# Kernel tuning notes

Hardware: AMD Instinct MI355X
Metric: run time of the kernel (lower is better)

## Reference

```python
import jax, jax.numpy as jnp
import numpy as np

B, S, L2 = 1, 2048, 512
DIM, HEADS, HD, FFN = 1536, 12, 128, 8960
BLK, TOPK, EPS = 64, 8, 1e-6
SCALE = HD ** -0.5

def _ln(x):
    xc = x - jnp.mean(x, -1, keepdims=True)
    return xc * jax.lax.rsqrt(jnp.mean(xc * xc, -1, keepdims=True) + EPS)

def _rms(x, w):
    return x * jax.lax.rsqrt(jnp.mean(x * x, -1, keepdims=True) + EPS) * w

def _rope(x, cos, sin):
    # is_neox_style=False: interleaved pairs
    x1, x2 = x[..., 0::2], x[..., 1::2]
    c, s = cos[None, :, None, :], sin[None, :, None, :]
    return jnp.stack([x1 * c - x2 * s, x2 * c + x1 * s], -1).reshape(x.shape)

def forward(hidden_states, encoder_hidden_states, temb, cos, sin, scale_shift_table,
            Wq, bq, Wk, bk, Wv, bv, Wg, bg, Wo, bo, qnorm_w, knorm_w, sa_ln_w, sa_ln_b,
            cWq, cbq, cWk, cbk, cWv, cbv, cWo, cbo, cqnorm_w, cknorm_w, W1, b1, W2, b2):
    e = scale_shift_table + temb  # [B,6,DIM]
    shift_msa, scale_msa, gate_msa = e[:, 0:1], e[:, 1:2], e[:, 2:3]
    c_shift, c_scale, c_gate = e[:, 3:4], e[:, 4:5], e[:, 5:6]
    norm_hs = _ln(hidden_states) * (1.0 + scale_msa) + shift_msa
    q = _rms(norm_hs @ Wq + bq, qnorm_w).reshape(B, S, HEADS, HD)
    k = _rms(norm_hs @ Wk + bk, knorm_w).reshape(B, S, HEADS, HD)
    v = (norm_hs @ Wv + bv).reshape(B, S, HEADS, HD)
    g = (norm_hs @ Wg + bg).reshape(B, S, HEADS, HD)  # gate_compress
    q, k = _rope(q, cos, sin), _rope(k, cos, sin)
    # ---- Video Sparse Attention: coarse (gated) branch + block top-k fine branch ----
    nb = S // BLK
    qc = q.reshape(B, nb, BLK, HEADS, HD).mean(2)  # cube-pooled
    kc = k.reshape(B, nb, BLK, HEADS, HD).mean(2)
    vc = v.reshape(B, nb, BLK, HEADS, HD).mean(2)
    pc = jax.nn.softmax(jnp.einsum('bnhd,bmhd->bhnm', qc, kc) * SCALE, -1)
    coarse = jnp.repeat(jnp.einsum('bhnm,bmhd->bnhd', pc, vc), BLK, axis=1)  # [B,S,H,D]
    _, idx = jax.lax.top_k(pc, TOPK)  # [B,H,nb,TOPK] selected kv blocks
    blk_mask = jax.nn.one_hot(idx, nb, dtype=jnp.float32).sum(-2) > 0  # [B,H,nb,nb]
    tok_mask = jnp.repeat(jnp.repeat(blk_mask, BLK, 2), BLK, 3)  # [B,H,S,S]
    s_fine = jnp.einsum('bshd,bthd->bhst', q, k) * SCALE
    p = jax.nn.softmax(jnp.where(tok_mask, s_fine, -1e9), -1)
    fine = jnp.einsum('bhst,bthd->bshd', p, v)
    attn = (fine + g * coarse).reshape(B, S, DIM) @ Wo + bo
    # ---- ScaleResidualLayerNormScaleShift (affine LN, null shift/scale) ----
    res = hidden_states + gate_msa * attn
    norm2 = _ln(res) * sa_ln_w + sa_ln_b
    # ---- WanT2VCrossAttention ----
    cq = _rms(norm2 @ cWq + cbq, cqnorm_w).reshape(B, S, HEADS, HD)
    ck = _rms(encoder_hidden_states @ cWk + cbk, cknorm_w).reshape(B, L2, HEADS, HD)
    cv = (encoder_hidden_states @ cWv + cbv).reshape(B, L2, HEADS, HD)
    cp = jax.nn.softmax(jnp.einsum('bshd,bthd->bhst', cq, ck) * SCALE, -1)
    cross = jnp.einsum('bhst,bthd->bshd', cp, cv).reshape(B, S, DIM) @ cWo + cbo
    res2 = res + cross
    norm3 = _ln(res2) * (1.0 + c_scale) + c_shift  # non-affine LN + scale-shift
    # ---- gelu-tanh MLP + gated residual ----
    ff = jax.nn.gelu(norm3 @ W1 + b1, approximate=True) @ W2 + b2
    return res2 + c_gate * ff

def setup_inputs():
    key = jax.random.key(0)
    ks = jax.random.split(key, 16)
    def w(i, shape, s=0.02):
        return jax.random.normal(ks[i], shape, jnp.float32) * s
    ang = jnp.arange(S, dtype=jnp.float32)[:, None] / (10000.0 ** (jnp.arange(0, HD, 2, dtype=jnp.float32) / HD))[None, :]
    z = lambda n: jnp.zeros((n,), jnp.float32)
    o = lambda n: jnp.ones((n,), jnp.float32)
    return {
        'hidden_states': jax.random.normal(ks[0], (B, S, DIM), jnp.float32),
        'encoder_hidden_states': jax.random.normal(ks[1], (B, L2, DIM), jnp.float32),
        'temb': jax.random.normal(ks[2], (B, 6, DIM), jnp.float32),
        'cos': jnp.cos(ang), 'sin': jnp.sin(ang),
        'scale_shift_table': jax.random.normal(ks[3], (1, 6, DIM), jnp.float32) / DIM ** 0.5,
        'Wq': w(4, (DIM, DIM)), 'bq': z(DIM), 'Wk': w(5, (DIM, DIM)), 'bk': z(DIM),
        'Wv': w(6, (DIM, DIM)), 'bv': z(DIM), 'Wg': w(7, (DIM, DIM)), 'bg': z(DIM),
        'Wo': w(8, (DIM, DIM)), 'bo': z(DIM),
        'qnorm_w': o(DIM), 'knorm_w': o(DIM), 'sa_ln_w': o(DIM), 'sa_ln_b': z(DIM),
        'cWq': w(9, (DIM, DIM)), 'cbq': z(DIM), 'cWk': w(10, (DIM, DIM)), 'cbk': z(DIM),
        'cWv': w(11, (DIM, DIM)), 'cbv': z(DIM), 'cWo': w(12, (DIM, DIM)), 'cbo': z(DIM),
        'cqnorm_w': o(DIM), 'cknorm_w': o(DIM),
        'W1': w(13, (DIM, FFN)), 'b1': z(FFN), 'W2': w(14, (FFN, DIM)), 'b2': z(DIM),
    }

def reference(hidden_states, encoder_hidden_states, temb, cos, sin, scale_shift_table, Wq, bq, Wk, bk, Wv, bv, Wg, bg, Wo, bo, qnorm_w, knorm_w, sa_ln_w, sa_ln_b, cWq, cbq, cWk, cbk, cWv, cbv, cWo, cbo, cqnorm_w, cknorm_w, W1, b1, W2, b2):
    return forward(hidden_states, encoder_hidden_states, temb, cos, sin, scale_shift_table, Wq, bq, Wk, bk, Wv, bv, Wg, bg, Wo, bo, qnorm_w, knorm_w, sa_ln_w, sa_ln_b, cWq, cbq, cWk, cbk, cWv, cbv, cWo, cbo, cqnorm_w, cknorm_w, W1, b1, W2, b2)
```

## Files before the change

### kernel.cpp

```cpp
#include <hip/hip_runtime.h>
#include <hip/hip_bf16.h>
#include <math.h>

#define DIMX 1536
#define SEQ 2048
#define L2X 512
#define NHEAD 12
#define HDIM 128
#define NBLK 32
#define FFNX 8960
#define SCALE_ATT 0.08838834764831845f

typedef __attribute__((ext_vector_type(4))) float f4;
typedef __attribute__((ext_vector_type(4))) float f32x4;
typedef __attribute__((ext_vector_type(8))) short bf16x8;
typedef __attribute__((ext_vector_type(4))) unsigned short us4;
typedef __attribute__((ext_vector_type(8))) unsigned short us8;
typedef unsigned short us;

static __device__ __forceinline__ us f2bf(float f) {
  union { float f; unsigned u; } v; v.f = f;
  unsigned r = v.u + 0x7FFFu + ((v.u >> 16) & 1u);
  return (us)(r >> 16);
}

static __device__ __forceinline__ void gl_lds16(const us* g, us* l) {
  __builtin_amdgcn_global_load_lds(
      (const __attribute__((address_space(1))) void*)g,
      (__attribute__((address_space(3))) void*)l, 16, 0, 0);
}

#define RAW_BAR() asm volatile("s_barrier" ::: "memory")

static __device__ __forceinline__ void xcd_map2(int& bx, int& by) {
  int gx = gridDim.x, gy = gridDim.y;
  int nwg = gx * gy;
  int lin = by * gx + bx;
  int q = nwg >> 3;
  lin = (lin & 7) * q + (lin >> 3);
  bx = lin % gx;
  by = lin / gx;
}

__global__ void __launch_bounds__(256) prep_e_kernel(const float* __restrict__ sst,
                                                     const float* __restrict__ temb,
                                                     float* __restrict__ e) {
  int i = blockIdx.x * 256 + threadIdx.x;
  if (i < 6 * DIMX) e[i] = sst[i] + temb[i];
}

struct P9 { const float* s[9]; };

__global__ void __launch_bounds__(256) pack64_9(P9 ps, us* __restrict__ dst) {
  const float* __restrict__ W = ps.s[blockIdx.z];
  us* __restrict__ Wt = dst + (size_t)blockIdx.z * DIMX * DIMX;
  __shared__ float t[64][65];
  int n0 = blockIdx.x * 64, k0 = blockIdx.y * 64;
  int tid = threadIdx.x;
#pragma unroll
  for (int i = 0; i < 4; i++) {
    int c = i * 256 + tid;
    int row = c >> 4, c4 = (c & 15) * 4;
    *reinterpret_cast<f4*>(&t[row][c4]) =
        *reinterpret_cast<const f4*>(&W[(size_t)(k0 + row) * DIMX + n0 + c4]);
  }
  __syncthreads();
#pragma unroll
  for (int i = 0; i < 2; i++) {
    int c = i * 256 + tid;
    int n = c >> 3, kc = (c & 7) * 8;
    us8 h;
#pragma unroll
    for (int j = 0; j < 8; j++) h[j] = f2bf(t[kc + j][n]);
    *reinterpret_cast<us8*>(&Wt[(size_t)(n0 + n) * DIMX + k0 + kc]) = h;
  }
}

__global__ void __launch_bounds__(256) pack64_g(const float* __restrict__ W,
                                                us* __restrict__ Wt, int K, int N) {
  __shared__ float t[64][65];
  int n0 = blockIdx.x * 64, k0 = blockIdx.y * 64;
  int tid = threadIdx.x;
#pragma unroll
  for (int i = 0; i < 4; i++) {
    int c = i * 256 + tid;
    int row = c >> 4, c4 = (c & 15) * 4;
    *reinterpret_cast<f4*>(&t[row][c4]) =
        *reinterpret_cast<const f4*>(&W[(size_t)(k0 + row) * N + n0 + c4]);
  }
  __syncthreads();
#pragma unroll
  for (int i = 0; i < 2; i++) {
    int c = i * 256 + tid;
    int n = c >> 3, kc = (c & 7) * 8;
    us8 h;
#pragma unroll
    for (int j = 0; j < 8; j++) h[j] = f2bf(t[kc + j][n]);
    *reinterpret_cast<us8*>(&Wt[(size_t)(n0 + n) * K + k0 + kc]) = h;
  }
}

__global__ void __launch_bounds__(256) pack_cvt_kernel(const float* __restrict__ X,
                                                       us* __restrict__ Y, int n4) {
  int i = blockIdx.x * 256 + threadIdx.x;
  if (i < n4) {
    f4 v = *reinterpret_cast<const f4*>(&X[(size_t)i * 4]);
    us4 h; h[0] = f2bf(v[0]); h[1] = f2bf(v[1]); h[2] = f2bf(v[2]); h[3] = f2bf(v[3]);
    *reinterpret_cast<us4*>(&Y[(size_t)i * 4]) = h;
  }
}

__global__ void __launch_bounds__(256) ln_affine_kernel(
    const float* __restrict__ X, const float* __restrict__ a,
    const float* __restrict__ b, int add1, us* __restrict__ Out) {
  __shared__ float lds4[4];
  int row = blockIdx.x, t = threadIdx.x;
  const float* x = X + (size_t)row * DIMX;
  float v[6]; float s = 0.f;
#pragma unroll
  for (int i = 0; i < 6; i++) { v[i] = x[t + 256 * i]; s += v[i]; }
  for (int o = 1; o < 64; o <<= 1) s += __shfl_xor(s, o, 64);
  if ((t & 63) == 0) lds4[t >> 6] = s;
  __syncthreads();
  float mean = (lds4[0] + lds4[1] + lds4[2] + lds4[3]) * (1.f / DIMX);
  __syncthreads();
  float s2 = 0.f;
#pragma unroll
  for (int i = 0; i < 6; i++) { float c = v[i] - mean; s2 += c * c; }
  for (int o = 1; o < 64; o <<= 1) s2 += __shfl_xor(s2, o, 64);
  if ((t & 63) == 0) lds4[t >> 6] = s2;
  __syncthreads();
  float var = (lds4[0] + lds4[1] + lds4[2] + lds4[3]) * (1.f / DIMX);
  float rstd = rsqrtf(var + 1e-6f);
#pragma unroll
  for (int i = 0; i < 6; i++) {
    int c = t + 256 * i;
    float av = a[c] + (add1 ? 1.f : 0.f);
    Out[(size_t)row * DIMX + c] = f2bf((v[i] - mean) * rstd * av + b[c]);
  }
}

__global__ void __launch_bounds__(256) reduce_ln_kernel(
    const float* __restrict__ P, const float* __restrict__ bias,
    const float* __restrict__ R, const float* __restrict__ g,
    float* __restrict__ Ores, const float* __restrict__ a,
    const float* __restrict__ b, int add1, us* __restrict__ Onorm) {
  __shared__ float lds4[4];
  int row = blockIdx.x, t = threadIdx.x;
  const size_t RN = (size_t)SEQ * DIMX;
  float v[6]; float s = 0.f;
#pragma unroll
  for (int i = 0; i < 6; i++) {
    int c = t + 256 * i;
    size_t ix = (size_t)row * DIMX + c;
    float x = P[ix];
    x += P[RN + ix]; x += P[2 * RN + ix]; x += P[3 * RN + ix];
    x += bias[c];
    x = g ? (R[ix] + g[c] * x) : (R[ix] + x);
    Ores[ix] = x;
    v[i] = x; s += x;
  }
  for (int o = 1; o < 64; o <<= 1) s += __shfl_xor(s, o, 64);
  if ((t & 63) == 0) lds4[t >> 6] = s;
  __syncthreads();
  float mean = (lds4[0] + lds4[1] + lds4[2] + lds4[3]) * (1.f / DIMX);
  __syncthreads();
  float s2 = 0.f;
#pragma unroll
  for (int i = 0; i < 6; i++) { float c = v[i] - mean; s2 += c * c; }
  for (int o = 1; o < 64; o <<= 1) s2 += __shfl_xor(s2, o, 64);
  if ((t & 63) == 0) lds4[t >> 6] = s2;
  __syncthreads();
  float var = (lds4[0] + lds4[1] + lds4[2] + lds4[3]) * (1.f / DIMX);
  float rstd = rsqrtf(var + 1e-6f);
#pragma unroll
  for (int i = 0; i < 6; i++) {
    int c = t + 256 * i;
    float av = a[c] + (add1 ? 1.f : 0.f);
    Onorm[(size_t)row * DIMX + c] = f2bf((v[i] - mean) * rstd * av + b[c]);
  }
}

__global__ void __launch_bounds__(256) rms_rope2_kernel(
    float* __restrict__ X0, float* __restrict__ X1,
    const float* __restrict__ w0, const float* __restrict__ w1,
    const float* __restrict__ cosT, const float* __restrict__ sinT, int do_rope,
    us* __restrict__ O0, us* __restrict__ O1) {
  __shared__ float lds4[4];
  int row = blockIdx.x, t = threadIdx.x;
  float* x = (blockIdx.y ? X1 : X0) + (size_t)row * DIMX;
  const float* wgt = blockIdx.y ? w1 : w0;
  us* Ob = blockIdx.y ? O1 : O0;
  int base = t * 6;
  float v[6]; float s2 = 0.f;
#pragma unroll
  for (int i = 0; i < 6; i++) { v[i] = x[base + i]; s2 += v[i] * v[i]; }
  for (int o = 1; o < 64; o <<= 1) s2 += __shfl_xor(s2, o, 64);
  if ((t & 63) == 0) lds4[t >> 6] = s2;
  __syncthreads();
  float ms = (lds4[0] + lds4[1] + lds4[2] + lds4[3]) * (1.f / DIMX);
  float rstd = rsqrtf(ms + 1e-6f);
#pragma unroll
  for (int i = 0; i < 6; i++) v[i] *= rstd * wgt[base + i];
  if (do_rope) {
#pragma unroll
    for (int j = 0; j < 3; j++) {
      int c = base + 2 * j;
      int pi = (c & (HDIM - 1)) >> 1;
      float cs = cosT[row * (HDIM / 2) + pi], sn = sinT[row * (HDIM / 2) + pi];
      float ev = v[2 * j], ov = v[2 * j + 1];
      v[2 * j] = ev * cs - ov * sn;
      v[2 * j + 1] = ov * cs + ev * sn;
    }
  }
#pragma unroll
  for (int i = 0; i < 6; i++) {
    x[base + i] = v[i];
    Ob[(size_t)row * DIMX + base + i] = f2bf(v[i]);
  }
}

__global__ void __launch_bounds__(256) rms_rope_kernel(
    float* __restrict__ X, const float* __restrict__ wgt,
    const float* __restrict__ cosT, const float* __restrict__ sinT, int do_rope,
    us* __restrict__ Ob) {
  __shared__ float lds4[4];
  int row = blockIdx.x, t = threadIdx.x;
  float* x = X + (size_t)row * DIMX;
  int base = t * 6;
  float v[6]; float s2 = 0.f;
#pragma unroll
  for (int i = 0; i < 6; i++) { v[i] = x[base + i]; s2 += v[i] * v[i]; }
  for (int o = 1; o < 64; o <<= 1) s2 += __shfl_xor(s2, o, 64);
  if ((t & 63) == 0) lds4[t >> 6] = s2;
  __syncthreads();
  float ms = (lds4[0] + lds4[1] + lds4[2] + lds4[3]) * (1.f / DIMX);
  float rstd = rsqrtf(ms + 1e-6f);
#pragma unroll
  for (int i = 0; i < 6; i++) v[i] *= rstd * wgt[base + i];
  if (do_rope) {
#pragma unroll
    for (int j = 0; j < 3; j++) {
      int c = base + 2 * j;
      int pi = (c & (HDIM - 1)) >> 1;
      float cs = cosT[row * (HDIM / 2) + pi], sn = sinT[row * (HDIM / 2) + pi];
      float ev = v[2 * j], ov = v[2 * j + 1];
      v[2 * j] = ev * cs - ov * sn;
      v[2 * j + 1] = ov * cs + ev * sn;
    }
  }
#pragma unroll
  for (int i = 0; i < 6; i++) {
    x[base + i] = v[i];
    Ob[(size_t)row * DIMX + base + i] = f2bf(v[i]);
  }
}

struct Outs {
  float *o0, *o1, *o2, *o3;
  const float *b0, *b1, *b2, *b3;
  us* ob;
};

template<int NP, int NCHUNK, int OUT_BF16, int DO_GELU, int SPLITK, int DIRECT>
__global__ void __launch_bounds__(512, 2) gemm2ph(
    const us* __restrict__ A, const us* __restrict__ Bt,
    Outs outs, int M, int N, int K, int Kfull) {
  constexpr int NT = NP * 32;
  constexpr int TOT = 16384 + NT * 64;
  constexpr int BI = (NT * 8 + 511) / 512;
  constexpr int NH0 = NP / 2;
  constexpr int NH1 = NP - NH0;
  __shared__ __align__(16) us S[2 * TOT];
  const int tid = threadIdx.x;
  const int lane = tid & 63;
  const int wid = tid >> 6;
  const int wr = wid >> 1, wc = wid & 1;
  const int fr = lane & 15, xo = lane >> 4;
  const int r7 = fr & 7, q4 = xo * 4;
  int tm, tn;
  if (DIRECT) {
    tm = blockIdx.x * 256; tn = blockIdx.y * NT;
  } else {
    int bx = blockIdx.x, by = blockIdx.y;
    xcd_map2(bx, by);
    tm = by * 256; tn = bx * NT;
  }
  const size_t kb = SPLITK ? (size_t)blockIdx.z * K : 0;

  auto stA = [&](int buf, int k0) {
#pragma unroll
    for (int i = 0; i < 4; i++) {
      int c = i * 512 + tid;
      gl_lds16(A + (size_t)(tm + (c >> 3)) * Kfull + kb + k0 + (((c & 7) ^ ((c >> 3) & 7)) * 8),
               S + buf * TOT + (i * 512 + wid * 64) * 8);
    }
  };
  auto stB = [&](int buf, int k0) {
#pragma unroll
    for (int i = 0; i < BI; i++) {
      int c = i * 512 + tid;
      if (c < NT * 8)
        gl_lds16(Bt + (size_t)(tn + (c >> 3)) * Kfull + kb + k0 + (((c & 7) ^ ((c >> 3) & 7)) * 8),
                 S + buf * TOT + 16384 + (i * 512 + wid * 64) * 8);
    }
  };
  auto rdA = [&](int buf, int mp, int ks) -> bf16x8 {
    int r = wr * 64 + mp * 16 + fr;
    int ko = ((ks * 4 + xo) ^ r7) * 8;
    return *reinterpret_cast<const bf16x8*>(&S[buf * TOT + r * 64 + ko]);
  };
  auto rdB = [&](int buf, int np, int ks) -> bf16x8 {
    int r = wc * (NP * 16) + np * 16 + fr;
    int ko = ((ks * 4 + xo) ^ r7) * 8;
    return *reinterpret_cast<const bf16x8*>(&S[buf * TOT + 16384 + r * 64 + ko]);
  };

  f32x4 acc[4][NP];
#pragma unroll
  for (int m = 0; m < 4; m++)
#pragma unroll
    for (int n = 0; n < NP; n++) acc[m][n] = (f32x4)(0.f);
  bf16x8 aF[2][4], bFr[2][NH1 > NH0 ? NH1 : NH0];

  const int nt = K >> 6;
  stA(0, 0); stB(0, 0); stA(1, 64);
  asm volatile("s_waitcnt vmcnt(4)" ::: "memory");
  RAW_BAR();

  for (int t = 0; t < nt; t++) {
    const int buf = t & 1;
    const int k1 = (t + 1) << 6, k2 = (t + 2) << 6;
#pragma unroll
    for (int ks = 0; ks < 2; ks++)
#pragma unroll
      for (int m = 0; m < 4; m++) aF[ks][m] = rdA(buf, m, ks);
#pragma unroll
    for (int ks = 0; ks < 2; ks++)
#pragma unroll
      for (int n = 0; n < NH0; n++) bFr[ks][n] = rdB(buf, n, ks);
    if (t + 1 < nt) stB(buf ^ 1, k1);
    RAW_BAR();
    __builtin_amdgcn_s_setprio(1);
#pragma unroll
    for (int ks = 0; ks < 2; ks++)
#pragma unroll
      for (int m = 0; m < 4; m++)
#pragma unroll
        for (int n = 0; n < NH0; n++)
          acc[m][n] = __builtin_amdgcn_mfma_f32_16x16x32_bf16(aF[ks][m], bFr[ks][n], acc[m][n], 0, 0, 0);
    __builtin_amdgcn_s_setprio(0);
    RAW_BAR();
#pragma unroll
    for (int ks = 0; ks < 2; ks++)
#pragma unroll
      for (int n = 0; n < NH1; n++) bFr[ks][n] = rdB(buf, NH0 + n, ks);
    if (t + 2 < nt) stA(buf, k2);
    RAW_BAR();
    __builtin_amdgcn_s_setprio(1);
#pragma unroll
    for (int ks = 0; ks < 2; ks++)
#pragma unroll
      for (int m = 0; m < 4; m++)
#pragma unroll
        for (int n = 0; n < NH1; n++)
          acc[m][NH0 + n] = __builtin_amdgcn_mfma_f32_16x16x32_bf16(aF[ks][m], bFr[ks][n], acc[m][NH0 + n], 0, 0, 0);
    __builtin_amdgcn_s_setprio(0);
    if (t + 2 < nt) asm volatile("s_waitcnt vmcnt(4)" ::: "memory");
    else            asm volatile("s_waitcnt vmcnt(0)" ::: "memory");
    RAW_BAR();
  }

#pragma unroll
  for (int m = 0; m < 4; m++)
#pragma unroll
    for (int n = 0; n < NP; n++) {
      int col = tn + wc * (NP * 16) + n * 16 + fr;
      int rowb = tm + wr * 64 + m * 16 + q4;
      if (SPLITK) {
        float* P = outs.o0 + (size_t)blockIdx.z * M * N;
#pragma unroll
        for (int r = 0; r < 4; r++)
          P[(size_t)(rowb + r) * N + col] = acc[m][n][r];
      } else {
        int c2; float* op; const float* bp; int sel = 0;
        if constexpr (NCHUNK == 1) {
          c2 = col; op = outs.o0; bp = outs.b0;
        } else {
          sel = col >= 3 * DIMX ? 3 : (col >= 2 * DIMX ? 2 : (col >= DIMX ? 1 : 0));
          c2 = col - sel * DIMX;
          op = sel == 0 ? outs.o0 : (sel == 1 ? outs.o1 : (sel == 2 ? outs.o2 : outs.o3));
          bp = sel == 0 ? outs.b0 : (sel == 1 ? outs.b1 : (sel == 2 ? outs.b2 : outs.b3));
        }
        float bv = bp[c2];
#pragma unroll
        for (int r = 0; r < 4; r++) {
          float v = acc[m][n][r] + bv;
          if (DO_GELU) {
            float u = 1.5957691216057308f * (v + 0.044715f * v * v * v);
            v = v / (1.f + __expf(-u));
          }
          if (OUT_BF16)
            outs.ob[(size_t)(rowb + r) * N + col] = f2bf(v);
          else {
            op[(size_t)(rowb + r) * DIMX + c2] = v;
            if (NCHUNK == 4 && outs.ob != nullptr && sel == 2)
              outs.ob[(size_t)(rowb + r) * DIMX + c2] = f2bf(v);
          }
        }
      }
    }
}

__global__ void __launch_bounds__(512, 2) gemm10(
    const us* __restrict__ A, const us* __restrict__ Bt,
    const float* __restrict__ bias, us* __restrict__ Cb,
    int M, int N, int K) {
  constexpr int NT = 320;
  constexpr int TOT = 16384 + NT * 64;
  __shared__ __align__(16) us S[2 * TOT];
  const int tid = threadIdx.x;
  const int lane = tid & 63;
  const int wid = tid >> 6;
  const int wr = wid >> 2, wc = wid & 3;
  const int fr = lane & 15, xo = lane >> 4;
  const int r7 = fr & 7, q4 = xo * 4;
  const int tm = blockIdx.x * 256, tn = blockIdx.y * NT;

  auto stA = [&](int buf, int k0) {
#pragma unroll
    for (int i = 0; i < 4; i++) {
      int c = i * 512 + tid;
      gl_lds16(A + (size_t)(tm + (c >> 3)) * K + k0 + (((c & 7) ^ ((c >> 3) & 7)) * 8),
               S + buf * TOT + (i * 512 + wid * 64) * 8);
    }
  };
  auto stB = [&](int buf, int k0) {
#pragma unroll
    for (int i = 0; i < 5; i++) {
      int c = i * 512 + tid;
      gl_lds16(Bt + (size_t)(tn + (c >> 3)) * K + k0 + (((c & 7) ^ ((c >> 3) & 7)) * 8),
               S + buf * TOT + 16384 + (i * 512 + wid * 64) * 8);
    }
  };
  auto rdA = [&](int buf, int mp, int ks) -> bf16x8 {
    int r = wr * 128 + mp * 16 + fr;
    int ko = ((ks * 4 + xo) ^ r7) * 8;
    return *reinterpret_cast<const bf16x8*>(&S[buf * TOT + r * 64 + ko]);
  };
  auto rdB = [&](int buf, int np, int ks) -> bf16x8 {
    int r = wc * 80 + np * 16 + fr;
    int ko = ((ks * 4 + xo) ^ r7) * 8;
    return *reinterpret_cast<const bf16x8*>(&S[buf * TOT + 16384 + r * 64 + ko]);
  };

  f32x4 acc[8][5];
#pragma unroll
  for (int m = 0; m < 8; m++)
#pragma unroll
    for (int n = 0; n < 5; n++) acc[m][n] = (f32x4)(0.f);
  bf16x8 aF[8], bF[5];

  const int nt = K >> 6;
  stA(0, 0); stB(0, 0); stA(1, 64);
  asm volatile("s_waitcnt vmcnt(4)" ::: "memory");
  RAW_BAR();

  for (int t = 0; t < nt; t++) {
    const int buf = t & 1;
    const int k1 = (t + 1) << 6, k2 = (t + 2) << 6;
#pragma unroll
    for (int m = 0; m < 8; m++) aF[m] = rdA(buf, m, 0);
#pragma unroll
    for (int n = 0; n < 5; n++) bF[n] = rdB(buf, n, 0);
    if (t + 1 < nt) stB(buf ^ 1, k1);
    RAW_BAR();
    __builtin_amdgcn_s_setprio(1);
#pragma unroll
    for (int m = 0; m < 8; m++)
#pragma unroll
      for (int n = 0; n < 5; n++)
        acc[m][n] = __builtin_amdgcn_mfma_f32_16x16x32_bf16(aF[m], bF[n], acc[m][n], 0, 0, 0);
    __builtin_amdgcn_s_setprio(0);
    RAW_BAR();
#pragma unroll
    for (int m = 0; m < 8; m++) aF[m] = rdA(buf, m, 1);
#pragma unroll
    for (int n = 0; n < 5; n++) bF[n] = rdB(buf, n, 1);
    if (t + 2 < nt) stA(buf, k2);
    RAW_BAR();
    __builtin_amdgcn_s_setprio(1);
#pragma unroll
    for (int m = 0; m < 8; m++)
#pragma unroll
      for (int n = 0; n < 5; n++)
        acc[m][n] = __builtin_amdgcn_mfma_f32_16x16x32_bf16(aF[m], bF[n], acc[m][n], 0, 0, 0);
    __builtin_amdgcn_s_setprio(0);
    if (t + 2 < nt) asm volatile("s_waitcnt vmcnt(4)" ::: "memory");
    else            asm volatile("s_waitcnt vmcnt(0)" ::: "memory");
    RAW_BAR();
  }

#pragma unroll
  for (int m = 0; m < 8; m++)
#pragma unroll
    for (int n = 0; n < 5; n++) {
      int col = tn + wc * 80 + n * 16 + fr;
      int rowb = tm + wr * 128 + m * 16 + q4;
      float bv = bias[col];
#pragma unroll
      for (int r = 0; r < 4; r++) {
        float v = acc[m][n][r] + bv;
        float u = 1.5957691216057308f * (v + 0.044715f * v * v * v);
        v = v / (1.f + __expf(-u));
        Cb[(size_t)(rowb + r) * N + col] = f2bf(v);
      }
    }
}

template<int NCHUNK>
__global__ void __launch_bounds__(256) gemm_multi(
    const us* __restrict__ A, const us* __restrict__ Bt,
    Outs outs, int M, int N, int K) {
  __shared__ __align__(16) us As[128 * 64];
  __shared__ __align__(16) us Bs[128 * 64];
  const int tid = threadIdx.x;
  const int lane = tid & 63;
  const int w = tid >> 6;
  const int wr = w >> 1, wc = w & 1;
  const int fr = lane & 15;
  const int xo = lane >> 4;
  const int r7 = fr & 7;
  const int q4 = xo * 4;
  int bx = blockIdx.x, by = blockIdx.y;
  xcd_map2(bx, by);
  const int tm = by * 128, tn = bx * 128;

  f32x4 acc[4][4];
#pragma unroll
  for (int m = 0; m < 4; m++)
#pragma unroll
    for (int n = 0; n < 4; n++) acc[m][n] = (f32x4)(0.f);

  int srow[4], skc[4];
#pragma unroll
  for (int j = 0; j < 4; j++) {
    int c = j * 256 + tid;
    srow[j] = c >> 3;
    skc[j] = ((c & 7) ^ ((c >> 3) & 7)) * 8;
  }

  for (int k0 = 0; k0 < K; k0 += 64) {
#pragma unroll
    for (int j = 0; j < 4; j++) {
      gl_lds16(A + (size_t)(tm + srow[j]) * K + k0 + skc[j], As + (j * 256 + w * 64) * 8);
      gl_lds16(Bt + (size_t)(tn + srow[j]) * K + k0 + skc[j], Bs + (j * 256 + w * 64) * 8);
    }
    __syncthreads();
    bf16x8 af[2][4], bfv[2][4];
#pragma unroll
    for (int ks = 0; ks < 2; ks++) {
      const int koff = (((ks * 4 + xo) ^ r7) << 3);
#pragma unroll
      for (int m = 0; m < 4; m++)
        af[ks][m] = *reinterpret_cast<const bf16x8*>(&As[(wr * 64 + m * 16 + fr) * 64 + koff]);
#pragma unroll
      for (int n = 0; n < 4; n++)
        bfv[ks][n] = *reinterpret_cast<const bf16x8*>(&Bs[(wc * 64 + n * 16 + fr) * 64 + koff]);
    }
#pragma unroll
    for (int ks = 0; ks < 2; ks++)
#pragma unroll
      for (int m = 0; m < 4; m++)
#pragma unroll
        for (int n = 0; n < 4; n++)
          acc[m][n] = __builtin_amdgcn_mfma_f32_16x16x32_bf16(af[ks][m], bfv[ks][n], acc[m][n], 0, 0, 0);
    __syncthreads();
  }
#pragma unroll
  for (int m = 0; m < 4; m++) {
#pragma unroll
    for (int n = 0; n < 4; n++) {
      int col = tn + wc * 64 + n * 16 + fr;
      int c2; float* op; const float* bp;
      if constexpr (NCHUNK == 2) {
        int sel = col >= DIMX;
        c2 = col - sel * DIMX;
        op = sel ? outs.o1 : outs.o0;
        bp = sel ? outs.b1 : outs.b0;
      } else {
        c2 = col; op = outs.o0; bp = outs.b0;
      }
      float bv = bp[c2];
#pragma unroll
      for (int r = 0; r < 4; r++) {
        int row = tm + wr * 64 + m * 16 + q4 + r;
        op[(size_t)row * DIMX + c2] = acc[m][n][r] + bv;
      }
    }
  }
}

template<int S>
__global__ void __launch_bounds__(256) reduce_kernel(
    const float* __restrict__ P, const float* __restrict__ bias,
    const float* __restrict__ R, const float* __restrict__ g,
    float* __restrict__ O, int total4, int ncol4) {
  const f4* P4 = (const f4*)P;
  const f4* R4 = (const f4*)R;
  f4* O4 = (f4*)O;
  for (int i = blockIdx.x * 256 + threadIdx.x; i < total4; i += gridDim.x * 256) {
    f4 s = P4[i];
#pragma unroll
    for (int sl = 1; sl < S; sl++) s += P4[(size_t)sl * total4 + i];
    int c4 = (i % ncol4) * 4;
    s += *reinterpret_cast<const f4*>(&bias[c4]);
    if (R) {
      if (g) {
        f4 gv = *reinterpret_cast<const f4*>(&g[c4]);
        s = R4[i] + gv * s;
      } else {
        s = R4[i] + s;
      }
    }
    O4[i] = s;
  }
}

__global__ void __launch_bounds__(256) attn_kernel(
    const us* __restrict__ Q, const us* __restrict__ Kx,
    const us* __restrict__ V, const int* __restrict__ idx,
    const float* __restrict__ G, const float* __restrict__ CB,
    us* __restrict__ Out) {
  __shared__ us k_s[64 * 136];
  __shared__ us vT_s[128 * 72];
  __shared__ us p_s[4][16 * 72];

  const int qb = blockIdx.x;
  const int h = blockIdx.y;
  const int tid = threadIdx.x;
  const int lane = tid & 63;
  const int w = tid >> 6;
  const int fr = lane & 15;
  const int xo = lane >> 4;
  const int k8 = xo * 8;
  const int q4 = xo * 4;

  bf16x8 qF[4];
#pragma unroll
  for (int kk = 0; kk < 4; kk++)
    qF[kk] = *reinterpret_cast<const bf16x8*>(
        &Q[(size_t)(qb * 64 + w * 16 + fr) * DIMX + h * HDIM + kk * 32 + k8]);

  float m_[4], l_[4];
#pragma unroll
  for (int r = 0; r < 4; r++) { m_[r] = -1e30f; l_[r] = 0.f; }
  f32x4 acc[8];
#pragma unroll
  for (int n = 0; n < 8; n++) acc[n] = (f32x4)(0.f);

  for (int ib = 0; ib < 8; ib++) {
    int blk = idx ? idx[(h * NBLK + qb) * 8 + ib] : ib;
    __syncthreads();
#pragma unroll
    for (int i = 0; i < 4; i++) {
      int c = i * 256 + tid;
      int row = c >> 4, d8 = (c & 15) * 8;
      us8 v = *reinterpret_cast<const us8*>(&Kx[(size_t)(blk * 64 + row) * DIMX + h * HDIM + d8]);
      *reinterpret_cast<us8*>(&k_s[row * 136 + d8]) = v;
    }
    {
      int d = tid & 127, th = (tid >> 7) * 32;
#pragma unroll
      for (int j = 0; j < 4; j++) {
        us8 hv;
#pragma unroll
        for (int qq = 0; qq < 8; qq++)
          hv[qq] = V[(size_t)(blk * 64 + th + j * 8 + qq) * DIMX + h * HDIM + d];
        *reinterpret_cast<us8*>(&vT_s[d * 72 + th + j * 8]) = hv;
      }
    }
    __syncthreads();
    f32x4 accs[4];
#pragma unroll
    for (int n = 0; n < 4; n++) accs[n] = (f32x4)(0.f);
#pragma unroll
    for (int kk = 0; kk < 4; kk++)
#pragma unroll
      for (int n = 0; n < 4; n++) {
        bf16x8 kb = *reinterpret_cast<const bf16x8*>(&k_s[(n * 16 + fr) * 136 + kk * 32 + k8]);
        accs[n] = __builtin_amdgcn_mfma_f32_16x16x32_bf16(qF[kk], kb, accs[n], 0, 0, 0);
      }
#pragma unroll
    for (int n = 0; n < 4; n++)
#pragma unroll
      for (int r = 0; r < 4; r++) accs[n][r] *= SCALE_ATT;
    float al[4];
#pragma unroll
    for (int r = 0; r < 4; r++) {
      float v = fmaxf(fmaxf(accs[0][r], accs[1][r]), fmaxf(accs[2][r], accs[3][r]));
      for (int o = 1; o < 16; o <<= 1) v = fmaxf(v, __shfl_xor(v, o, 64));
      float mn = fmaxf(m_[r], v);
      al[r] = __expf(m_[r] - mn);
      m_[r] = mn;
      l_[r] *= al[r];
    }
    float ps[4] = {0.f, 0.f, 0.f, 0.f};
#pragma unroll
    for (int n = 0; n < 4; n++)
#pragma unroll
      for (int r = 0; r < 4; r++) {
        float p = __expf(accs[n][r] - m_[r]);
        p_s[w][(q4 + r) * 72 + n * 16 + fr] = f2bf(p);
        ps[r] += p;
      }
#pragma unroll
    for (int r = 0; r < 4; r++) {
      float sv = ps[r];
      for (int o = 1; o < 16; o <<= 1) sv += __shfl_xor(sv, o, 64);
      l_[r] += sv;
    }
#pragma unroll
    for (int n = 0; n < 8; n++) {
      acc[n][0] *= al[0]; acc[n][1] *= al[1];
      acc[n][2] *= al[2]; acc[n][3] *= al[3];
    }
    bf16x8 pa[2];
#pragma unroll
    for (int ks = 0; ks < 2; ks++)
      pa[ks] = *reinterpret_cast<const bf16x8*>(&p_s[w][fr * 72 + ks * 32 + k8]);
#pragma unroll
    for (int ks = 0; ks < 2; ks++)
#pragma unroll
      for (int n = 0; n < 8; n++) {
        bf16x8 vb = *reinterpret_cast<const bf16x8*>(&vT_s[(n * 16 + fr) * 72 + ks * 32 + k8]);
        acc[n] = __builtin_amdgcn_mfma_f32_16x16x32_bf16(pa[ks], vb, acc[n], 0, 0, 0);
      }
  }
#pragma unroll
  for (int n = 0; n < 8; n++)
#pragma unroll
    for (int r = 0; r < 4; r++) {
      int srow = qb * 64 + w * 16 + q4 + r;
      int d = n * 16 + fr;
      float o = acc[n][r] / l_[r];
      size_t oi = (size_t)srow * DIMX + h * HDIM + d;
      if (G) o += G[oi] * CB[(size_t)qb * DIMX + h * HDIM + d];
      Out[oi] = f2bf(o);
    }
}

__global__ void __launch_bounds__(128) block_mean3_kernel(const float* __restrict__ q,
                                                          const float* __restrict__ k,
                                                          const float* __restrict__ v,
                                                          float* __restrict__ qc,
                                                          float* __restrict__ kc,
                                                          float* __restrict__ vc) {
  int n = blockIdx.x, h = blockIdx.y, z = blockIdx.z, d = threadIdx.x;
  const float* X = z == 0 ? q : (z == 1 ? k : v);
  float* O = z == 0 ? qc : (z == 1 ? kc : vc);
  float s = 0.f;
  for (int t = 0; t < 64; t++) s += X[(size_t)(n * 64 + t) * DIMX + h * HDIM + d];
  O[(n * NHEAD + h) * HDIM + d] = s * (1.f / 64.f);
}

__global__ void __launch_bounds__(256) coarse_attn_kernel(const float* __restrict__ qc,
                                                          const float* __restrict__ kc,
                                                          float* __restrict__ pc,
                                                          int* __restrict__ idxout) {
  int h = blockIdx.x, t = threadIdx.x;
  __shared__ float sm[32][32];
  for (int p = t; p < 1024; p += 256) {
    int n = p >> 5, m = p & 31;
    float dot = 0.f;
    for (int d = 0; d < HDIM; d++)
      dot += qc[n * DIMX + h * HDIM + d] * kc[m * DIMX + h * HDIM + d];
    sm[n][m] = dot * SCALE_ATT;
  }
  __syncthreads();
  if (t < 32) {
    int n = t;
    float mx = -1e30f;
#pragma unroll
    for (int m = 0; m < 32; m++) mx = fmaxf(mx, sm[n][m]);
    float pv[32]; float ssum = 0.f;
#pragma unroll
    for (int m = 0; m < 32; m++) { pv[m] = __expf(sm[n][m] - mx); ssum += pv[m]; }
    float inv = 1.f / ssum;
#pragma unroll
    for (int m = 0; m < 32; m++) { pv[m] *= inv; pc[(h * 32 + n) * 32 + m] = pv[m]; }
    unsigned chosen = 0;
    for (int i = 0; i < 8; i++) {
      float best = -1.f; int bi = 0;
#pragma unroll
      for (int m = 0; m < 32; m++)
        if (!((chosen >> m) & 1u) && pv[m] > best) { best = pv[m]; bi = m; }
      chosen |= 1u << bi;
      idxout[(h * 32 + n) * 8 + i] = bi;
    }
  }
}

__global__ void __launch_bounds__(128) coarse_ctx_kernel(const float* __restrict__ pc,
                                                         const float* __restrict__ vc,
                                                         float* __restrict__ cb) {
  int n = blockIdx.x, h = blockIdx.y, d = threadIdx.x;
  float s = 0.f;
  for (int m = 0; m < 32; m++)
    s += pc[(h * 32 + n) * 32 + m] * vc[(m * NHEAD + h) * HDIM + d];
  cb[(n * NHEAD + h) * HDIM + d] = s;
}

extern "C" void kernel_launch(void* const* d_in, const int* in_sizes, int n_in,
                              void* d_out, int out_size, void* d_ws, size_t ws_size,
                              hipStream_t stream) {
  (void)in_sizes; (void)n_in; (void)out_size; (void)ws_size;
  const float* hidden = (const float*)d_in[0];
  const float* enc    = (const float*)d_in[1];
  const float* temb   = (const float*)d_in[2];
  const float* cosT   = (const float*)d_in[3];
  const float* sinT   = (const float*)d_in[4];
  const float* sst    = (const float*)d_in[5];
  const float* Wq = (const float*)d_in[6];   const float* bq = (const float*)d_in[7];
  const float* Wk = (const float*)d_in[8];   const float* bk = (const float*)d_in[9];
  const float* Wv = (const float*)d_in[10];  const float* bv = (const float*)d_in[11];
  const float* Wg = (const float*)d_in[12];  const float* bg = (const float*)d_in[13];
  const float* Wo = (const float*)d_in[14];  const float* bo = (const float*)d_in[15];
  const float* qnw = (const float*)d_in[16]; const float* knw = (const float*)d_in[17];
  const float* saw = (const float*)d_in[18]; const float* sab = (const float*)d_in[19];
  const float* cWq = (const float*)d_in[20]; const float* cbq = (const float*)d_in[21];
  const float* cWk = (const float*)d_in[22]; const float* cbk = (const float*)d_in[23];
  const float* cWv = (const float*)d_in[24]; const float* cbv = (const float*)d_in[25];
  const float* cWo = (const float*)d_in[26]; const float* cbo = (const float*)d_in[27];
  const float* cqnw = (const float*)d_in[28]; const float* cknw = (const float*)d_in[29];
  const float* W1 = (const float*)d_in[30];  const float* b1 = (const float*)d_in[31];
  const float* W2 = (const float*)d_in[32];  const float* b2 = (const float*)d_in[33];

  char* ws = (char*)d_ws;
  size_t off = 0;
  auto alloc = [&](size_t bytes) -> void* {
    void* p = ws + off;
    off += (bytes + 255) & ~(size_t)255;
    return p;
  };
  const size_t SD = (size_t)SEQ * DIMX * 4;
  const size_t SDh = (size_t)SEQ * DIMX * 2;
  const size_t WSQ = (size_t)DIMX * DIMX * 2;
  float* e     = (float*)alloc(6 * DIMX * 4);
  us* normb    = (us*)alloc(SDh);
  float* qb_   = (float*)alloc(SD);
  float* kb_   = (float*)alloc(SD);
  float* vb_   = (float*)alloc(SD);
  float* gb_   = (float*)alloc(SD);
  us* qbh      = (us*)alloc(SDh);
  us* kbh      = (us*)alloc(SDh);
  us* vbh      = (us*)alloc(SDh);
  float* qc    = (float*)alloc((size_t)NBLK * DIMX * 4);
  float* kc    = (float*)alloc((size_t)NBLK * DIMX * 4);
  float* vc    = (float*)alloc((size_t)NBLK * DIMX * 4);
  float* pc    = (float*)alloc(NHEAD * 32 * 32 * 4);
  int*   idx   = (int*)alloc(NHEAD * 32 * 8 * 4);
  float* cb    = (float*)alloc((size_t)NBLK * DIMX * 4);
  us* mixb     = (us*)alloc(SDh);
  float* res   = (float*)alloc(SD);
  us* encb     = (us*)alloc((size_t)L2X * DIMX * 2);
  us* wpack    = (us*)alloc(9 * WSQ);
  us* W1t      = (us*)alloc((size_t)DIMX * FFNX * 2);
  us* W2t      = (us*)alloc((size_t)FFNX * DIMX * 2);
  us* ffh    = (us*)qb_;
  us* crossb = mixb;
  float* part4q = qb_;
  float* part4w = (float*)wpack;
  float* outf  = (float*)d_out;
  const size_t SL = (size_t)DIMX * DIMX;
  us* Wot  = wpack + 4 * SL;
  us* cWqt = wpack + 5 * SL;
  us* cKVt = wpack + 6 * SL;
  us* cWot = wpack + 8 * SL;

  P9 p9; p9.s[0]=Wq; p9.s[1]=Wk; p9.s[2]=Wv; p9.s[3]=Wg; p9.s[4]=Wo;
  p9.s[5]=cWq; p9.s[6]=cWk; p9.s[7]=cWv; p9.s[8]=cWo;
  pack64_9<<<dim3(DIMX / 64, DIMX / 64, 9), 256, 0, stream>>>(p9, wpack);
  pack64_g<<<dim3(FFNX / 64, DIMX / 64), 256, 0, stream>>>(W1, W1t, DIMX, FFNX);
  pack64_g<<<dim3(DIMX / 64, FFNX / 64), 256, 0, stream>>>(W2, W2t, FFNX, DIMX);
  pack_cvt_kernel<<<(L2X * DIMX / 4 + 255) / 256, 256, 0, stream>>>(enc, encb, L2X * DIMX / 4);
  prep_e_kernel<<<36, 256, 0, stream>>>(sst, temb, e);

  ln_affine_kernel<<<SEQ, 256, 0, stream>>>(hidden, e + DIMX, e, 1, normb);
  Outs qkvgo = {qb_, kb_, vb_, gb_, bq, bk, bv, bg, vbh};
  gemm2ph<6, 4, 0, 0, 0, 1><<<dim3(8, 32), 512, 0, stream>>>(normb, wpack, qkvgo, SEQ, 4 * DIMX, DIMX, DIMX);
  rms_rope2_kernel<<<dim3(SEQ, 2), 256, 0, stream>>>(qb_, kb_, qnw, knw, cosT, sinT, 1, qbh, kbh);
  block_mean3_kernel<<<dim3(NBLK, NHEAD, 3), 128, 0, stream>>>(qb_, kb_, vb_, qc, kc, vc);
  coarse_attn_kernel<<<NHEAD, 256, 0, stream>>>(qc, kc, pc, idx);
  coarse_ctx_kernel<<<dim3(NBLK, NHEAD), 128, 0, stream>>>(pc, vc, cb);
  attn_kernel<<<dim3(NBLK, NHEAD), 256, 0, stream>>>(qbh, kbh, vbh, idx, gb_, cb, mixb);
  Outs wo_o = {part4q, nullptr, nullptr, nullptr, nullptr, nullptr, nullptr, nullptr, nullptr};
  gemm2ph<6, 1, 0, 0, 1, 1><<<dim3(8, 8, 4), 512, 0, stream>>>(mixb, Wot, wo_o, SEQ, DIMX, 384, DIMX);
  reduce_ln_kernel<<<SEQ, 256, 0, stream>>>(part4q, bo, hidden, e + 2 * DIMX,
                                            res, saw, sab, 0, normb);
  gemm2ph<6, 1, 0, 0, 1, 1><<<dim3(8, 8, 4), 512, 0, stream>>>(normb, cWqt, wo_o, SEQ, DIMX, 384, DIMX);
  reduce_kernel<4><<<1024, 256, 0, stream>>>(part4q, cbq, nullptr, nullptr, qb_,
                                             SEQ * DIMX / 4, DIMX / 4);
  rms_rope_kernel<<<SEQ, 256, 0, stream>>>(qb_, cqnw, cosT, sinT, 0, qbh);
  Outs ckvo = {kb_, vb_, nullptr, nullptr, cbk, cbv, nullptr, nullptr, nullptr};
  gemm_multi<2><<<dim3(24, 4), 256, 0, stream>>>(encb, cKVt, ckvo, L2X, 2 * DIMX, DIMX);
  rms_rope_kernel<<<L2X, 256, 0, stream>>>(kb_, cknw, cosT, sinT, 0, kbh);
  pack_cvt_kernel<<<(L2X * DIMX / 4 + 255) / 256, 256, 0, stream>>>(vb_, vbh, L2X * DIMX / 4);
  attn_kernel<<<dim3(NBLK, NHEAD), 256, 0, stream>>>(qbh, kbh, vbh, nullptr, nullptr, nullptr, crossb);
  gemm2ph<6, 1, 0, 0, 1, 1><<<dim3(8, 8, 4), 512, 0, stream>>>(crossb, cWot, wo_o, SEQ, DIMX, 384, DIMX);
  reduce_ln_kernel<<<SEQ, 256, 0, stream>>>(part4q, cbo, res, nullptr,
                                            outf, e + 4 * DIMX, e + 3 * DIMX, 1, normb);
  gemm10<<<dim3(8, 28), 512, 0, stream>>>(normb, W1t, b1, ffh, SEQ, FFNX, DIMX);
  Outs f2o = {part4w, nullptr, nullptr, nullptr, nullptr, nullptr, nullptr, nullptr, nullptr};
  gemm2ph<6, 1, 0, 0, 1, 1><<<dim3(8, 8, 4), 512, 0, stream>>>(ffh, W2t, f2o, SEQ, DIMX, 2240, FFNX);
  reduce_kernel<4><<<1024, 256, 0, stream>>>(part4w, b2, outf, e + 5 * DIMX, outf,
                                             SEQ * DIMX / 4, DIMX / 4);
}
```

Before: 550.5 us.

## Fuse cross-attn Q reduce with RMSNorm, emit bf16 V in GEMM, prefetch attention tiles

The split-K reduction for the cross-attention Q projection is merged with its RMSNorm into one per-row kernel that writes bf16 directly. This removes a separate reduce kernel and an fp32 round trip. The cross K/V GEMM now writes the V half straight to bf16 in its epilogue, which drops a pack_cvt launch. The attention kernel also prefetches the next K/V tile into registers while computing the current block, trading extra register pressure for overlap of global loads with MFMA work.

```diff
diff --git a/kernel.cpp b/kernel.cpp
--- a/kernel.cpp
+++ b/kernel.cpp
@@ -178,6 +178,35 @@
     int c = t + 256 * i;
     float av = a[c] + (add1 ? 1.f : 0.f);
     Onorm[(size_t)row * DIMX + c] = f2bf((v[i] - mean) * rstd * av + b[c]);
+  }
+}
+
+__global__ void __launch_bounds__(256) reduce_rms_kernel(
+    const float* __restrict__ P, const float* __restrict__ bias,
+    const float* __restrict__ w, us* __restrict__ Ob) {
+  __shared__ float lds4[4];
+  int row = blockIdx.x, t = threadIdx.x;
+  const size_t RN = (size_t)SEQ * DIMX;
+  float v[6]; float s2 = 0.f;
+#pragma unroll
+  for (int i = 0; i < 6; i++) {
+    int c = t + 256 * i;
+    size_t ix = (size_t)row * DIMX + c;
+    float x = P[ix];
+    x += P[RN + ix]; x += P[2 * RN + ix]; x += P[3 * RN + ix];
+    x += bias[c];
+    v[i] = x; s2 += x * x;
+  }
+  for (int o = 1; o < 64; o <<= 1) s2 += __shfl_xor(s2, o, 64);
+  if ((t & 63) == 0) lds4[t >> 6] = s2;
+  __syncthreads();
+  float ms = (lds4[0] + lds4[1] + lds4[2] + lds4[3]) * (1.f / DIMX);
+  float rstd = rsqrtf(ms + 1e-6f);
+#pragma unroll
+  for (int i = 0; i < 6; i++) {
+    int c = t + 256 * i;
+    float y = v[i] * (rstd * w[c]);
+    Ob[(size_t)row * DIMX + c] = f2bf(y);
   }
 }
 
@@ -582,9 +611,9 @@
 #pragma unroll
     for (int n = 0; n < 4; n++) {
       int col = tn + wc * 64 + n * 16 + fr;
-      int c2; float* op; const float* bp;
+      int c2; float* op; const float* bp; int sel = 0;
       if constexpr (NCHUNK == 2) {
-        int sel = col >= DIMX;
+        sel = col >= DIMX;
         c2 = col - sel * DIMX;
         op = sel ? outs.o1 : outs.o0;
         bp = sel ? outs.b1 : outs.b0;
@@ -595,7 +624,11 @@
 #pragma unroll
       for (int r = 0; r < 4; r++) {
         int row = tm + wr * 64 + m * 16 + q4 + r;
-        op[(size_t)row * DIMX + c2] = acc[m][n][r] + bv;
+        float v = acc[m][n][r] + bv;
+        if (NCHUNK == 2 && outs.ob != nullptr && sel == 1)
+          outs.ob[(size_t)row * DIMX + c2] = f2bf(v);
+        else
+          op[(size_t)row * DIMX + c2] = v;
       }
     }
   }
@@ -645,6 +678,7 @@
   const int xo = lane >> 4;
   const int k8 = xo * 8;
   const int q4 = xo * 4;
+  const int vd = tid & 127, vth = (tid >> 7) * 32;
 
   bf16x8 qF[4];
 #pragma unroll
@@ -652,35 +686,52 @@
     qF[kk] = *reinterpret_cast<const bf16x8*>(
         &Q[(size_t)(qb * 64 + w * 16 + fr) * DIMX + h * HDIM + kk * 32 + k8]);
 
-  float m_[4], l_[4];
-#pragma unroll
-  for (int r = 0; r < 4; r++) { m_[r] = -1e30f; l_[r] = 0.f; }
-  f32x4 acc[8];
-#pragma unroll
-  for (int n = 0; n < 8; n++) acc[n] = (f32x4)(0.f);
-
-  for (int ib = 0; ib < 8; ib++) {
-    int blk = idx ? idx[(h * NBLK + qb) * 8 + ib] : ib;
-    __syncthreads();
+  us8 kR[4], vR[4];
+  auto loadTile = [&](int blk) {
 #pragma unroll
     for (int i = 0; i < 4; i++) {
       int c = i * 256 + tid;
       int row = c >> 4, d8 = (c & 15) * 8;
-      us8 v = *reinterpret_cast<const us8*>(&Kx[(size_t)(blk * 64 + row) * DIMX + h * HDIM + d8]);
-      *reinterpret_cast<us8*>(&k_s[row * 136 + d8]) = v;
-    }
-    {
-      int d = tid & 127, th = (tid >> 7) * 32;
-#pragma unroll
-      for (int j = 0; j < 4; j++) {
-        us8 hv;
-#pragma unroll
-        for (int qq = 0; qq < 8; qq++)
-          hv[qq] = V[(size_t)(blk * 64 + th + j * 8 + qq) * DIMX + h * HDIM + d];
-        *reinterpret_cast<us8*>(&vT_s[d * 72 + th + j * 8]) = hv;
-      }
-    }
+      kR[i] = *reinterpret_cast<const us8*>(&Kx[(size_t)(blk * 64 + row) * DIMX + h * HDIM + d8]);
+    }
+#pragma unroll
+    for (int j = 0; j < 4; j++) {
+      us8 hv;
+#pragma unroll
+      for (int qq = 0; qq < 8; qq++)
+        hv[qq] = V[(size_t)(blk * 64 + vth + j * 8 + qq) * DIMX + h * HDIM + vd];
+      vR[j] = hv;
+    }
+  };
+
+  float m_[4], l_[4];
+#pragma unroll
+  for (int r = 0; r < 4; r++) { m_[r] = -1e30f; l_[r] = 0.f; }
+  f32x4 acc[8];
+#pragma unroll
+  for (int n = 0; n < 8; n++) acc[n] = (f32x4)(0.f);
+
+  {
+    int blk0 = idx ? idx[(h * NBLK + qb) * 8 + 0] : 0;
+    loadTile(blk0);
+  }
+
+  for (int ib = 0; ib < 8; ib++) {
     __syncthreads();
+#pragma unroll
+    for (int i = 0; i < 4; i++) {
+      int c = i * 256 + tid;
+      int row = c >> 4, d8 = (c & 15) * 8;
+      *reinterpret_cast<us8*>(&k_s[row * 136 + d8]) = kR[i];
+    }
+#pragma unroll
+    for (int j = 0; j < 4; j++)
+      *reinterpret_cast<us8*>(&vT_s[vd * 72 + vth + j * 8]) = vR[j];
+    __syncthreads();
+    if (ib + 1 < 8) {
+      int blkn = idx ? idx[(h * NBLK + qb) * 8 + ib + 1] : ib + 1;
+      loadTile(blkn);
+    }
     f32x4 accs[4];
 #pragma unroll
     for (int n = 0; n < 4; n++) accs[n] = (f32x4)(0.f);
@@ -899,13 +950,10 @@
   reduce_ln_kernel<<<SEQ, 256, 0, stream>>>(part4q, bo, hidden, e + 2 * DIMX,
                                             res, saw, sab, 0, normb);
   gemm2ph<6, 1, 0, 0, 1, 1><<<dim3(8, 8, 4), 512, 0, stream>>>(normb, cWqt, wo_o, SEQ, DIMX, 384, DIMX);
-  reduce_kernel<4><<<1024, 256, 0, stream>>>(part4q, cbq, nullptr, nullptr, qb_,
-                                             SEQ * DIMX / 4, DIMX / 4);
-  rms_rope_kernel<<<SEQ, 256, 0, stream>>>(qb_, cqnw, cosT, sinT, 0, qbh);
-  Outs ckvo = {kb_, vb_, nullptr, nullptr, cbk, cbv, nullptr, nullptr, nullptr};
+  reduce_rms_kernel<<<SEQ, 256, 0, stream>>>(part4q, cbq, cqnw, qbh);
+  Outs ckvo = {kb_, vb_, nullptr, nullptr, cbk, cbv, nullptr, nullptr, vbh};
   gemm_multi<2><<<dim3(24, 4), 256, 0, stream>>>(encb, cKVt, ckvo, L2X, 2 * DIMX, DIMX);
   rms_rope_kernel<<<L2X, 256, 0, stream>>>(kb_, cknw, cosT, sinT, 0, kbh);
-  pack_cvt_kernel<<<(L2X * DIMX / 4 + 255) / 256, 256, 0, stream>>>(vb_, vbh, L2X * DIMX / 4);
   attn_kernel<<<dim3(NBLK, NHEAD), 256, 0, stream>>>(qbh, kbh, vbh, nullptr, nullptr, nullptr, crossb);
   gemm2ph<6, 1, 0, 0, 1, 1><<<dim3(8, 8, 4), 512, 0, stream>>>(crossb, cWot, wo_o, SEQ, DIMX, 384, DIMX);
   reduce_ln_kernel<<<SEQ, 256, 0, stream>>>(part4q, cbo, res, nullptr,
```

Result: faster. 508.7 us (-7.6%).
